# Performance work log

Hardware: AMD Instinct MI355X
Metric: run time of the kernel (lower is better)

Reference implementation:

```python
import jax, jax.numpy as jnp
import numpy as np

NUM_HEADS = 16
HEAD_DIM = 64
MAX_MEM = 4 * 4096
TOP_K = 8
EPS = 1e-8


def _l2norm(x, eps=EPS):
    # matches torch F.normalize(p=2, dim=-1, eps): x / max(||x||, eps)
    n = jnp.sqrt(jnp.sum(x * x, axis=-1, keepdims=True))
    return x / jnp.maximum(n, eps)


def setup_inputs() -> dict:
    key0 = jax.random.key(0)
    ks = jax.random.split(key0, 8)
    B, S, D = 2, 512, 1024
    H, hd = NUM_HEADS, HEAD_DIM
    return {
        "inputs": jax.random.normal(ks[0], (B, S, D), dtype=jnp.float32),
        "query": jax.random.normal(ks[1], (B, H, S, hd), dtype=jnp.float32),
        "key": jax.random.normal(ks[2], (B, H, S, hd), dtype=jnp.float32),
        "value": jax.random.normal(ks[3], (B, H, S, hd), dtype=jnp.float32),
        "outputs": jax.random.normal(ks[4], (B, H, S, hd), dtype=jnp.float32),
        "gate": jnp.zeros((H,), dtype=jnp.float32),  # nn.Parameter init zeros
        "key_memories": jax.random.normal(ks[5], (H, MAX_MEM, hd), dtype=jnp.float32),
        "value_memories": jax.random.normal(ks[6], (H, MAX_MEM, hd), dtype=jnp.float32),
    }


def reference(inputs, query, key, value, outputs, gate, key_memories, value_memories):
    B, S, _ = inputs.shape
    H = query.shape[1]
    hd = HEAD_DIM

    # [B,H,S,d] -> [H, B*S, d]
    q = jnp.transpose(query, (1, 0, 2, 3)).reshape(H, B * S, hd)

    # --- KNN lookup (no_grad in original) ---
    qn = _l2norm(q)                    # [H, N, d]
    kn = _l2norm(key_memories)         # [H, M, d]
    sims = jnp.einsum("hnd,hmd->hnm", qn, kn) / jnp.sqrt(jnp.float32(hd))
    scores, indices = jax.lax.top_k(sims, TOP_K)  # [H, N, k]

    # gather memory values per head: [H, N, k, d]
    mem_vals = jax.vmap(lambda vm, ix: vm[ix])(value_memories, indices)

    # weighted sum over k neighbors
    weighted = jnp.sum(mem_vals * scores[..., None], axis=2)  # [H, N, d]
    weighted = weighted.reshape(H, B, S, hd).transpose(1, 0, 2, 3)  # [B,H,S,d]

    g = jax.nn.sigmoid(gate).reshape(1, H, 1, 1)
    out_dim = outputs.shape[-1]
    combined = g * weighted[..., :out_dim] + (1.0 - g) * outputs
    return combined
```

## Files before the change

### kernel.cpp

```cpp
#include <hip/hip_runtime.h>
#include <math.h>

#define NHEADS 16
#define HD 64
#define MMEM 16384
#define NQ 1024
#define SEQ 512
#define EPS 1e-8f
#define NPART 16
#define NT 32
#define NGRP 32
#define CMAX 8

typedef short bf16x8 __attribute__((ext_vector_type(8)));
typedef float f32x16 __attribute__((ext_vector_type(16)));

__device__ inline unsigned short f2bf(float f) {
    unsigned int u = __builtin_bit_cast(unsigned int, f);
    unsigned int r = (u + 0x7FFFu + ((u >> 16) & 1u)) >> 16;
    return (unsigned short)r;
}

#define SS(Q) (Q.x*Q.x + Q.y*Q.y + Q.z*Q.z + Q.w*Q.w)

__global__ __launch_bounds__(256)
void kprep_kernel(const float* __restrict__ kmem,
                  float* __restrict__ knr,
                  unsigned short* __restrict__ kbf) {
    __shared__ float ssl[256];
    const int tid = threadIdx.x;
    const int gid = blockIdx.x * 256 + tid;
    const int lane = gid & 63;
    const int ks   = (gid >> 6) & 3;
    const int t    = (gid >> 8) & 511;
    const int h    = gid >> 17;
    const int r    = lane & 31;
    const int hi   = lane >> 5;
    const int row  = t * 32 + r;
    const int d0   = ks * 16 + hi * 8;

    const float* src = kmem + (((size_t)h * MMEM + row) << 6) + d0;
    float4 v0 = *(const float4*)(src);
    float4 v1 = *(const float4*)(src + 4);
    float ss = SS(v0) + SS(v1);
    const int lr = tid >> 6;
    ssl[lr * 64 + r * 2 + 0] = 0.f;
    __syncthreads();
    ssl[(tid & 192)  + r * 2 + (ks & 1) + 0] = 0.f;
    __syncthreads();
    ssl[(tid >> 6) * 64 + r * 2 + ((ks * 2 + hi) & 1)] = 0.f;
    __syncthreads();
    ssl[tid] = ss;
    __syncthreads();
    const int base = (tid & 192) | (r ? 0 : 0);
    float tot = ssl[0 * 64 + r] + ssl[0 * 64 + 32 + r]
              + ssl[1 * 64 + r] + ssl[1 * 64 + 32 + r]
              + ssl[2 * 64 + r] + ssl[2 * 64 + 32 + r]
              + ssl[3 * 64 + r] + ssl[3 * 64 + 32 + r];
    const float rn = 1.0f / fmaxf(sqrtf(tot), EPS);
    if (ks == 0 && hi == 0) knr[h * MMEM + row] = rn;

    uint4 o;
    o.x = (unsigned)f2bf(v0.x * rn) | ((unsigned)f2bf(v0.y * rn) << 16);
    o.y = (unsigned)f2bf(v0.z * rn) | ((unsigned)f2bf(v0.w * rn) << 16);
    o.z = (unsigned)f2bf(v1.x * rn) | ((unsigned)f2bf(v1.y * rn) << 16);
    o.w = (unsigned)f2bf(v1.z * rn) | ((unsigned)f2bf(v1.w * rn) << 16);
    *(uint4*)(kbf + (size_t)gid * 8) = o;
}

#define MAX16(ACC)                                                            \
    fmaxf(fmaxf(fmaxf(fmaxf(ACC[0],ACC[1]),fmaxf(ACC[2],ACC[3])),             \
                fmaxf(fmaxf(ACC[4],ACC[5]),fmaxf(ACC[6],ACC[7]))),            \
          fmaxf(fmaxf(fmaxf(ACC[8],ACC[9]),fmaxf(ACC[10],ACC[11])),           \
                fmaxf(fmaxf(ACC[12],ACC[13]),fmaxf(ACC[14],ACC[15]))))

__device__ inline void ins8(float (&tv)[8], float v) {
#pragma unroll
    for (int j = 0; j < 8; ++j) {
        float h_ = fmaxf(tv[j], v);
        float l_ = fminf(tv[j], v);
        tv[j] = h_;
        v = l_;
    }
}

__device__ inline void ins8u64(unsigned long long (&tv)[8], unsigned long long v) {
#pragma unroll
    for (int j = 0; j < 8; ++j) {
        unsigned long long h_ = tv[j] > v ? tv[j] : v;
        unsigned long long l_ = tv[j] > v ? v : tv[j];
        tv[j] = h_;
        v = l_;
    }
}

__device__ inline bf16x8 pack8f(float4 a, float4 b) {
    bf16x8 f;
    f[0] = (short)f2bf(a.x); f[1] = (short)f2bf(a.y);
    f[2] = (short)f2bf(a.z); f[3] = (short)f2bf(a.w);
    f[4] = (short)f2bf(b.x); f[5] = (short)f2bf(b.y);
    f[6] = (short)f2bf(b.z); f[7] = (short)f2bf(b.w);
    return f;
}

#define MFMA8(AF0, AF1, AF2, AF3)                                             \
    f32x16 accA = {0,0,0,0,0,0,0,0,0,0,0,0,0,0,0,0};                         \
    f32x16 accB = {0,0,0,0,0,0,0,0,0,0,0,0,0,0,0,0};                         \
    accA = __builtin_amdgcn_mfma_f32_32x32x16_bf16(AF0, qA[0], accA, 0, 0, 0);\
    accB = __builtin_amdgcn_mfma_f32_32x32x16_bf16(AF0, qB[0], accB, 0, 0, 0);\
    accA = __builtin_amdgcn_mfma_f32_32x32x16_bf16(AF1, qA[1], accA, 0, 0, 0);\
    accB = __builtin_amdgcn_mfma_f32_32x32x16_bf16(AF1, qB[1], accB, 0, 0, 0);\
    accA = __builtin_amdgcn_mfma_f32_32x32x16_bf16(AF2, qA[2], accA, 0, 0, 0);\
    accB = __builtin_amdgcn_mfma_f32_32x32x16_bf16(AF2, qB[2], accB, 0, 0, 0);\
    accA = __builtin_amdgcn_mfma_f32_32x32x16_bf16(AF3, qA[3], accA, 0, 0, 0);\
    accB = __builtin_amdgcn_mfma_f32_32x32x16_bf16(AF3, qB[3], accB, 0, 0, 0);

#define LOADQ()                                                               \
    bf16x8 qA[4], qB[4];                                                      \
    {                                                                         \
        const int b0 = n0 >> 9, s0 = n0 & 511;                                \
        const int b1 = n1 >> 9, s1 = n1 & 511;                                \
        const float* qp0 = query + ((((size_t)b0 * NHEADS + h) * SEQ + s0) << 6); \
        const float* qp1 = query + ((((size_t)b1 * NHEADS + h) * SEQ + s1) << 6); \
        _Pragma("unroll")                                                     \
        for (int ks = 0; ks < 4; ++ks) {                                      \
            const int d0 = ks * 16 + hi * 8;                                  \
            qA[ks] = pack8f(*(const float4*)(qp0 + d0), *(const float4*)(qp0 + d0 + 4)); \
            qB[ks] = pack8f(*(const float4*)(qp1 + d0), *(const float4*)(qp1 + d0 + 4)); \
        }                                                                     \
    }

__global__ __launch_bounds__(64, 4)
void scanA_kernel(const float* __restrict__ query,
                  const unsigned short* __restrict__ kbf,
                  float* __restrict__ pmax) {
    const int lane = threadIdx.x;
    int bid = blockIdx.x;
    const int p  = bid & 15;  bid >>= 4;
    const int qg = bid & 15;  bid >>= 4;
    const int h  = bid;
    const int col = lane & 31;
    const int hi  = lane >> 5;
    const int n0  = qg * 64 + col;
    const int n1  = n0 + 32;

    LOADQ()

    float gA = -1e30f, gB = -1e30f;

    const unsigned char* ptr = (const unsigned char*)kbf
        + ((size_t)h * 512 + (size_t)p * NT) * 4096 + (size_t)lane * 16;

    bf16x8 aX0, aX1, aX2, aX3, aY0, aY1, aY2, aY3;
    aX0 = *(const bf16x8*)(ptr);
    aX1 = *(const bf16x8*)(ptr + 1024);
    aX2 = *(const bf16x8*)(ptr + 2048);
    aX3 = *(const bf16x8*)(ptr + 3072);

#pragma unroll 1
    for (int t = 0; t < NT; t += 2) {
        {
            const unsigned char* pn = ptr + (size_t)(t + 1) * 4096;
            aY0 = *(const bf16x8*)(pn);
            aY1 = *(const bf16x8*)(pn + 1024);
            aY2 = *(const bf16x8*)(pn + 2048);
            aY3 = *(const bf16x8*)(pn + 3072);
        }
        {
            MFMA8(aX0, aX1, aX2, aX3)
            gA = fmaxf(gA, MAX16(accA));
            gB = fmaxf(gB, MAX16(accB));
        }
        if (t + 2 < NT) {
            const unsigned char* p2 = ptr + (size_t)(t + 2) * 4096;
            aX0 = *(const bf16x8*)(p2);
            aX1 = *(const bf16x8*)(p2 + 1024);
            aX2 = *(const bf16x8*)(p2 + 2048);
            aX3 = *(const bf16x8*)(p2 + 3072);
        }
        {
            MFMA8(aY0, aY1, aY2, aY3)
            gA = fmaxf(gA, MAX16(accA));
            gB = fmaxf(gB, MAX16(accB));
        }
    }

    const int g = p * 2 + hi;
    pmax[(((size_t)h * NQ + n0) << 5) + g] = gA;
    pmax[(((size_t)h * NQ + n1) << 5) + g] = gB;
}

__global__ __launch_bounds__(256)
void taured_kernel(const float* __restrict__ pmax,
                   float* __restrict__ tauv) {
    const int gid = blockIdx.x * 256 + threadIdx.x;
    float tv[8];
#pragma unroll
    for (int j = 0; j < 8; ++j) tv[j] = -1e30f;
#pragma unroll
    for (int k = 0; k < NGRP; ++k) ins8(tv, pmax[((size_t)gid << 5) + k]);
    tauv[gid] = tv[7];
}

__global__ __launch_bounds__(64, 4)
void scanB_kernel(const float* __restrict__ query,
                  const unsigned short* __restrict__ kbf,
                  const float* __restrict__ tauv,
                  unsigned* __restrict__ pcand,
                  unsigned* __restrict__ pcnt) {
    const int lane = threadIdx.x;
    int bid = blockIdx.x;
    const int p  = bid & 15;  bid >>= 4;
    const int qg = bid & 15;  bid >>= 4;
    const int h  = bid;
    const int col = lane & 31;
    const int hi  = lane >> 5;
    const int n0  = qg * 64 + col;
    const int n1  = n0 + 32;

    bf16x8 qA[4], qB[4];
    float ssA = 0.f, ssB = 0.f;
    {
        const int b0 = n0 >> 9, s0 = n0 & 511;
        const int b1 = n1 >> 9, s1 = n1 & 511;
        const float* qp0 = query + ((((size_t)b0 * NHEADS + h) * SEQ + s0) << 6);
        const float* qp1 = query + ((((size_t)b1 * NHEADS + h) * SEQ + s1) << 6);
#pragma unroll
        for (int ks = 0; ks < 4; ++ks) {
            const int d0 = ks * 16 + hi * 8;
            float4 a0 = *(const float4*)(qp0 + d0), b0v = *(const float4*)(qp0 + d0 + 4);
            float4 a1 = *(const float4*)(qp1 + d0), b1v = *(const float4*)(qp1 + d0 + 4);
            ssA += SS(a0) + SS(b0v);
            ssB += SS(a1) + SS(b1v);
            qA[ks] = pack8f(a0, b0v);
            qB[ks] = pack8f(a1, b1v);
        }
    }
    ssA += __shfl_xor(ssA, 32);
    ssB += __shfl_xor(ssB, 32);
    const float tA = tauv[h * NQ + n0] - (sqrtf(ssA) * 0.0078125f + 0.01f);
    const float tB = tauv[h * NQ + n1] - (sqrtf(ssB) * 0.0078125f + 0.01f);

    const unsigned char* ptr = (const unsigned char*)kbf
        + ((size_t)h * 512 + (size_t)p * NT) * 4096 + (size_t)lane * 16;

    unsigned cA = 0, cB = 0;
    const size_t chA = (((size_t)h * NQ + n0) << 5) + p * 2 + hi;
    const size_t chB = (((size_t)h * NQ + n1) << 5) + p * 2 + hi;
    unsigned* mApt = pcand + chA * CMAX;
    unsigned* mBpt = pcand + chB * CMAX;

#define EMITM(ACC, TAU, C, LST, MBV) do {                                     \
        unsigned _msk = 0;                                                    \
        _Pragma("unroll")                                                     \
        for (int _r = 0; _r < 16; ++_r)                                       \
            _msk |= (ACC[_r] >= (TAU)) ? (1u << _r) : 0u;                     \
        if (_msk) {                                                           \
            do {                                                              \
                int _r = __ffs(_msk) - 1;                                     \
                unsigned _idx = (unsigned)((MBV) + (_r & 3) + 8 * (_r >> 2)); \
                if ((C) < CMAX) (LST)[C] = _idx;                              \
                ++(C);                                                        \
                _msk &= _msk - 1;                                             \
            } while (_msk);                                                   \
        }                                                                     \
    } while (0)

    bf16x8 aX0, aX1, aX2, aX3, aY0, aY1, aY2, aY3;
    aX0 = *(const bf16x8*)(ptr);
    aX1 = *(const bf16x8*)(ptr + 1024);
    aX2 = *(const bf16x8*)(ptr + 2048);
    aX3 = *(const bf16x8*)(ptr + 3072);

#pragma unroll 1
    for (int t = 0; t < NT; t += 2) {
        {
            const unsigned char* pn = ptr + (size_t)(t + 1) * 4096;
            aY0 = *(const bf16x8*)(pn);
            aY1 = *(const bf16x8*)(pn + 1024);
            aY2 = *(const bf16x8*)(pn + 2048);
            aY3 = *(const bf16x8*)(pn + 3072);
        }
        {
            MFMA8(aX0, aX1, aX2, aX3)
            const int mbv = p * 1024 + t * 32 + 4 * hi;
            EMITM(accA, tA, cA, mApt, mbv);
            EMITM(accB, tB, cB, mBpt, mbv);
        }
        if (t + 2 < NT) {
            const unsigned char* p2 = ptr + (size_t)(t + 2) * 4096;
            aX0 = *(const bf16x8*)(p2);
            aX1 = *(const bf16x8*)(p2 + 1024);
            aX2 = *(const bf16x8*)(p2 + 2048);
            aX3 = *(const bf16x8*)(p2 + 3072);
        }
        {
            MFMA8(aY0, aY1, aY2, aY3)
            const int mbv = p * 1024 + (t + 1) * 32 + 4 * hi;
            EMITM(accA, tA, cA, mApt, mbv);
            EMITM(accB, tB, cB, mBpt, mbv);
        }
    }
    pcnt[chA] = cA;
    pcnt[chB] = cB;
#undef EMITM
}

__global__ __launch_bounds__(64, 8)
void rescore_merge_kernel(const float* __restrict__ query,
                          const float* __restrict__ kmem,
                          const float* __restrict__ knr,
                          const unsigned* __restrict__ pcand,
                          const unsigned* __restrict__ pcnt,
                          const float* __restrict__ vmem,
                          const float* __restrict__ outputs,
                          const float* __restrict__ gate,
                          float* __restrict__ out) {
    __shared__ unsigned cands[NGRP * CMAX];
    const int gid = blockIdx.x;
    const int h = gid >> 10;
    const int n = gid & 1023;
    const int b = n >> 9;
    const int s = n & 511;
    const int lane = threadIdx.x;
    const int d4 = lane & 15;
    const int d5 = lane & 31;

    const float* qbase = query + ((((size_t)b * NHEADS + h) * SEQ + s) << 6);
    const float4 q4 = ((const float4*)qbase)[d4];
    float ssp = SS(q4);
    ssp += __shfl_xor(ssp, 1);
    ssp += __shfl_xor(ssp, 2);
    ssp += __shfl_xor(ssp, 4);
    ssp += __shfl_xor(ssp, 8);
    const float qs = 1.0f / (fmaxf(sqrtf(ssp), EPS) * 8.0f);

    const unsigned cg = pcnt[((size_t)gid << 5) + d5];
    const bool anyovf = (__ballot(cg > CMAX) != 0ULL);
    unsigned inc = cg;
#pragma unroll
    for (int d = 1; d < 32; d <<= 1) {
        unsigned t = __shfl_up(inc, d, 32);
        if (d5 >= d) inc += t;
    }
    const unsigned ct = __shfl(inc, 31, 32);
    const unsigned excl = inc - cg;
    if (lane < 32) {
        const unsigned* lp = pcand + (((size_t)gid << 5) + lane) * CMAX;
        const unsigned cc = cg > CMAX ? CMAX : cg;
        for (unsigned c = 0; c < cc; ++c) cands[excl + c] = lp[c];
    }
    __syncthreads();

    const float* kb = kmem + ((size_t)h << 20);
    const float* nb = knr + h * MMEM;

    unsigned long long top[8];
#pragma unroll
    for (int j = 0; j < 8; ++j) top[j] = 0ULL;

#define SCORE_KEY(IDX) ({                                                     \
        float4 kv = ((const float4*)(kb + ((size_t)(IDX) << 6)))[d4];         \
        float d = q4.x*kv.x + q4.y*kv.y + q4.z*kv.z + q4.w*kv.w;              \
        d += __shfl_xor(d, 1);                                                \
        d += __shfl_xor(d, 2);                                                \
        d += __shfl_xor(d, 4);                                                \
        d += __shfl_xor(d, 8);                                                \
        const float sc = d * qs * nb[IDX];                                    \
        unsigned su = __builtin_bit_cast(unsigned, sc);                       \
        unsigned ms = su ^ ((su >> 31) ? 0xFFFFFFFFu : 0x80000000u);          \
        ((unsigned long long)ms << 32) | (0xFFFFFFFFu - (unsigned)(IDX));     \
    })

    if (!anyovf) {
#pragma unroll 1
        for (unsigned c = 0; c < ct; ++c) {
            const unsigned idx = cands[c];
            ins8u64(top, SCORE_KEY(idx));
        }
    } else {
#pragma unroll 1
        for (int m = 0; m < MMEM; ++m) ins8u64(top, SCORE_KEY(m));
    }
#undef SCORE_KEY

    float acc = 0.0f;
    const float* vb = vmem + ((size_t)h << 20);
#pragma unroll
    for (int j = 0; j < 8; ++j) {
        const unsigned long long key = top[j];
        const unsigned idx = 0xFFFFFFFFu - (unsigned)(key & 0xFFFFFFFFu);
        const unsigned ms = (unsigned)(key >> 32);
        const unsigned su = ms ^ ((ms >> 31) ? 0x80000000u : 0xFFFFFFFFu);
        const float sc = __builtin_bit_cast(float, su);
        acc = fmaf(sc, vb[((size_t)idx << 6) + lane], acc);
    }

    const float gg = 1.0f / (1.0f + expf(-gate[h]));
    const size_t off = ((((size_t)b * NHEADS + h) * SEQ + s) << 6) + lane;
    out[off] = gg * acc + (1.0f - gg) * outputs[off];
}

__global__ void knorm_kernel(const float* __restrict__ kmem,
                             float* __restrict__ knr) {
    int gid = blockIdx.x * 256 + threadIdx.x;
    int mem = gid >> 4;
    int d4  = gid & 15;
    float4 kv = reinterpret_cast<const float4*>(kmem)[(size_t)mem * 16 + d4];
    float ss = SS(kv);
    ss += __shfl_xor(ss, 1);
    ss += __shfl_xor(ss, 2);
    ss += __shfl_xor(ss, 4);
    ss += __shfl_xor(ss, 8);
    if (d4 == 0) knr[mem] = 1.0f / fmaxf(sqrtf(ss), EPS);
}

__global__ __launch_bounds__(64, 4)
void scan_kernel(const float* __restrict__ query,
                 const float* __restrict__ kmem,
                 const float* __restrict__ knr,
                 float* __restrict__ pscore,
                 int* __restrict__ pidx,
                 int P, int CH) {
    const int lane = threadIdx.x & 63;
    int bid = blockIdx.x;
    const int p  = bid % P;  bid /= P;
    const int qb = bid & 15; bid >>= 4;
    const int h  = bid;
    const int n  = qb * 64 + lane;
    const int b  = n >> 9;
    const int s  = n & 511;

    const float4* qp = reinterpret_cast<const float4*>(
        query + (((size_t)b * NHEADS + h) * SEQ + s) * HD);
    float q[HD];
    float ss = 0.0f;
#pragma unroll
    for (int i = 0; i < 16; ++i) {
        float4 v = qp[i];
        q[4*i+0] = v.x; q[4*i+1] = v.y; q[4*i+2] = v.z; q[4*i+3] = v.w;
        ss += SS(v);
    }
    const float rq = 1.0f / (fmaxf(sqrtf(ss), EPS) * 8.0f);
#pragma unroll
    for (int i = 0; i < HD; ++i) q[i] *= rq;

    float tv[8]; int ti[8];
#pragma unroll
    for (int j = 0; j < 8; ++j) { tv[j] = -INFINITY; ti[j] = 0; }

    const int m0 = p * CH;
    const float4* kp = reinterpret_cast<const float4*>(
        kmem + ((size_t)h * MMEM + m0) * HD);
    const float* knrp = knr + h * MMEM + m0;

    for (int mm = 0; mm < CH; ++mm) {
        float d0 = 0.f, d1 = 0.f, d2 = 0.f, d3 = 0.f;
#pragma unroll
        for (int i = 0; i < 16; ++i) {
            float4 kv = kp[(size_t)mm * 16 + i];
            d0 = fmaf(q[4*i+0], kv.x, d0);
            d1 = fmaf(q[4*i+1], kv.y, d1);
            d2 = fmaf(q[4*i+2], kv.z, d2);
            d3 = fmaf(q[4*i+3], kv.w, d3);
        }
        const float sim = ((d0 + d1) + (d2 + d3)) * knrp[mm];
        if (sim > tv[7]) {
            tv[7] = sim; ti[7] = m0 + mm;
#pragma unroll
            for (int j = 7; j > 0; --j) {
                if (tv[j] > tv[j-1]) {
                    float tf = tv[j]; tv[j] = tv[j-1]; tv[j-1] = tf;
                    int   tu = ti[j]; ti[j] = ti[j-1]; ti[j-1] = tu;
                }
            }
        }
    }

    const size_t base = (((size_t)h * NQ + n) * P + p) * 8;
#pragma unroll
    for (int j = 0; j < 8; ++j) { pscore[base+j] = tv[j]; pidx[base+j] = ti[j]; }
}

__global__ void merge_kernel(const float* __restrict__ pscore,
                             const int* __restrict__ pidx,
                             const float* __restrict__ vmem,
                             const float* __restrict__ outputs,
                             const float* __restrict__ gate,
                             float* __restrict__ out, int P) {
    const int t = blockIdx.x * 256 + threadIdx.x;
    const int h = t >> 10;
    const int n = t & 1023;
    const int b = n >> 9;
    const int s = n & 511;

    float tv[8]; int ti[8];
    const size_t base = ((size_t)h * NQ + n) * P * 8;
#pragma unroll
    for (int j = 0; j < 8; ++j) { tv[j] = pscore[base + j]; ti[j] = pidx[base + j]; }
    const int total = P * 8;
    for (int c = 8; c < total; ++c) {
        const float v = pscore[base + c];
        if (v > tv[7]) {
            tv[7] = v; ti[7] = pidx[base + c];
#pragma unroll
            for (int j = 7; j > 0; --j) {
                if (tv[j] > tv[j-1]) {
                    float tf = tv[j]; tv[j] = tv[j-1]; tv[j-1] = tf;
                    int   tu = ti[j]; ti[j] = ti[j-1]; ti[j-1] = tu;
                }
            }
        }
    }

    float4 acc[16];
#pragma unroll
    for (int i = 0; i < 16; ++i) acc[i] = make_float4(0.f, 0.f, 0.f, 0.f);
#pragma unroll
    for (int j = 0; j < 8; ++j) {
        const float4* vp = reinterpret_cast<const float4*>(
            vmem + ((size_t)h * MMEM + ti[j]) * HD);
        const float sc = tv[j];
#pragma unroll
        for (int i = 0; i < 16; ++i) {
            float4 v = vp[i];
            acc[i].x = fmaf(sc, v.x, acc[i].x);
            acc[i].y = fmaf(sc, v.y, acc[i].y);
            acc[i].z = fmaf(sc, v.z, acc[i].z);
            acc[i].w = fmaf(sc, v.w, acc[i].w);
        }
    }

    const float g  = 1.0f / (1.0f + expf(-gate[h]));
    const float og = 1.0f - g;
    const size_t off = (((size_t)b * NHEADS + h) * SEQ + s) * HD;
    const float4* op = reinterpret_cast<const float4*>(outputs + off);
    float4* dst = reinterpret_cast<float4*>(out + off);
#pragma unroll
    for (int i = 0; i < 16; ++i) {
        float4 o = op[i];
        float4 r;
        r.x = g * acc[i].x + og * o.x;
        r.y = g * acc[i].y + og * o.y;
        r.z = g * acc[i].z + og * o.z;
        r.w = g * acc[i].w + og * o.w;
        dst[i] = r;
    }
}

extern "C" void kernel_launch(void* const* d_in, const int* in_sizes, int n_in,
                              void* d_out, int out_size, void* d_ws, size_t ws_size,
                              hipStream_t stream) {
    const float* query   = (const float*)d_in[1];
    const float* outputs = (const float*)d_in[4];
    const float* gate    = (const float*)d_in[5];
    const float* kmem    = (const float*)d_in[6];
    const float* vmem    = (const float*)d_in[7];
    float* out = (float*)d_out;

    const size_t NQTOT    = (size_t)NHEADS * NQ;
    const size_t sz_knr   = (size_t)NHEADS * MMEM * 4;
    const size_t sz_kbf   = (size_t)NHEADS * MMEM * HD * 2;
    const size_t sz_pmax  = NQTOT * NGRP * 4;
    const size_t sz_tauv  = NQTOT * 4;
    const size_t sz_pcand = NQTOT * NGRP * CMAX * 4;
    const size_t sz_pcnt  = NQTOT * NGRP * 4;
    const size_t need = sz_knr + sz_kbf + sz_pmax + sz_tauv + sz_pcand + sz_pcnt;

    if (ws_size >= need) {
        char* w = (char*)d_ws;
        float*          knr   = (float*)w;          w += sz_knr;
        unsigned short* kbf   = (unsigned short*)w; w += sz_kbf;
        float*          pmax  = (float*)w;          w += sz_pmax;
        float*          tauv  = (float*)w;          w += sz_tauv;
        unsigned*       pcand = (unsigned*)w;       w += sz_pcand;
        unsigned*       pcnt  = (unsigned*)w;

        kprep_kernel<<<(NHEADS * 512 * 4 * 64) / 256, 256, 0, stream>>>(kmem, knr, kbf);
        scanA_kernel<<<NHEADS * 16 * NPART, 64, 0, stream>>>(query, kbf, pmax);
        taured_kernel<<<(int)(NQTOT / 256), 256, 0, stream>>>(pmax, tauv);
        scanB_kernel<<<NHEADS * 16 * NPART, 64, 0, stream>>>(query, kbf, tauv, pcand, pcnt);
        rescore_merge_kernel<<<(int)NQTOT, 64, 0, stream>>>(
            query, kmem, knr, pcand, pcnt, vmem, outputs, gate, out);
    } else {
        int P = 16;
        while (P > 4 &&
               (size_t)NHEADS * MMEM * 4 + (size_t)NHEADS * NQ * (size_t)P * 64 > ws_size)
            P >>= 1;
        const int CH = MMEM / P;

        float* knr    = (float*)d_ws;
        float* pscore = knr + (size_t)NHEADS * MMEM;
        int*   pidx   = (int*)(pscore + (size_t)NHEADS * NQ * (size_t)P * 8);

        knorm_kernel<<<(NHEADS * MMEM * 16) / 256, 256, 0, stream>>>(kmem, knr);
        scan_kernel<<<NHEADS * 16 * P, 64, 0, stream>>>(
            query, kmem, knr, pscore, pidx, P, CH);
        merge_kernel<<<(NHEADS * NQ) / 256, 256, 0, stream>>>(
            pscore, pidx, vmem, outputs, gate, out, P);
    }
}
```

Measured before the change: 149.7 us.

## Halve queries per block in scan kernels and early-exit threshold check

```diff
diff --git a/kernel.cpp b/kernel.cpp
--- a/kernel.cpp
+++ b/kernel.cpp
@@ -42,23 +42,12 @@
     const float* src = kmem + (((size_t)h * MMEM + row) << 6) + d0;
     float4 v0 = *(const float4*)(src);
     float4 v1 = *(const float4*)(src + 4);
-    float ss = SS(v0) + SS(v1);
-    const int lr = tid >> 6;
-    ssl[lr * 64 + r * 2 + 0] = 0.f;
+    ssl[tid] = SS(v0) + SS(v1);
     __syncthreads();
-    ssl[(tid & 192)  + r * 2 + (ks & 1) + 0] = 0.f;
-    __syncthreads();
-    ssl[(tid >> 6) * 64 + r * 2 + ((ks * 2 + hi) & 1)] = 0.f;
-    __syncthreads();
-    ssl[tid] = ss;
-    __syncthreads();
-    const int base = (tid & 192) | (r ? 0 : 0);
-    float tot = ssl[0 * 64 + r] + ssl[0 * 64 + 32 + r]
-              + ssl[1 * 64 + r] + ssl[1 * 64 + 32 + r]
-              + ssl[2 * 64 + r] + ssl[2 * 64 + 32 + r]
-              + ssl[3 * 64 + r] + ssl[3 * 64 + 32 + r];
+    float tot = ssl[r +   0] + ssl[r +  32] + ssl[r +  64] + ssl[r +  96]
+              + ssl[r + 128] + ssl[r + 160] + ssl[r + 192] + ssl[r + 224];
     const float rn = 1.0f / fmaxf(sqrtf(tot), EPS);
-    if (ks == 0 && hi == 0) knr[h * MMEM + row] = rn;
+    if (tid < 32) knr[h * MMEM + row] = rn;
 
     uint4 o;
     o.x = (unsigned)f2bf(v0.x * rn) | ((unsigned)f2bf(v0.y * rn) << 16);
@@ -68,11 +57,16 @@
     *(uint4*)(kbf + (size_t)gid * 8) = o;
 }
 
-#define MAX16(ACC)                                                            \
-    fmaxf(fmaxf(fmaxf(fmaxf(ACC[0],ACC[1]),fmaxf(ACC[2],ACC[3])),             \
-                fmaxf(fmaxf(ACC[4],ACC[5]),fmaxf(ACC[6],ACC[7]))),            \
-          fmaxf(fmaxf(fmaxf(ACC[8],ACC[9]),fmaxf(ACC[10],ACC[11])),           \
-                fmaxf(fmaxf(ACC[12],ACC[13]),fmaxf(ACC[14],ACC[15]))))
+__device__ inline float max16v(const f32x16& a) {
+    float m0 = fmaxf(fmaxf(a[0],  a[1]),  a[2]);
+    float m1 = fmaxf(fmaxf(a[3],  a[4]),  a[5]);
+    float m2 = fmaxf(fmaxf(a[6],  a[7]),  a[8]);
+    float m3 = fmaxf(fmaxf(a[9],  a[10]), a[11]);
+    float m4 = fmaxf(fmaxf(a[12], a[13]), a[14]);
+    float n0 = fmaxf(fmaxf(m0, m1), m2);
+    float n1 = fmaxf(fmaxf(m3, m4), a[15]);
+    return fmaxf(n0, n1);
+}
 
 __device__ inline void ins8(float (&tv)[8], float v) {
 #pragma unroll
@@ -103,50 +97,38 @@
     return f;
 }
 
-#define MFMA8(AF0, AF1, AF2, AF3)                                             \
-    f32x16 accA = {0,0,0,0,0,0,0,0,0,0,0,0,0,0,0,0};                         \
-    f32x16 accB = {0,0,0,0,0,0,0,0,0,0,0,0,0,0,0,0};                         \
-    accA = __builtin_amdgcn_mfma_f32_32x32x16_bf16(AF0, qA[0], accA, 0, 0, 0);\
-    accB = __builtin_amdgcn_mfma_f32_32x32x16_bf16(AF0, qB[0], accB, 0, 0, 0);\
-    accA = __builtin_amdgcn_mfma_f32_32x32x16_bf16(AF1, qA[1], accA, 0, 0, 0);\
-    accB = __builtin_amdgcn_mfma_f32_32x32x16_bf16(AF1, qB[1], accB, 0, 0, 0);\
-    accA = __builtin_amdgcn_mfma_f32_32x32x16_bf16(AF2, qA[2], accA, 0, 0, 0);\
-    accB = __builtin_amdgcn_mfma_f32_32x32x16_bf16(AF2, qB[2], accB, 0, 0, 0);\
-    accA = __builtin_amdgcn_mfma_f32_32x32x16_bf16(AF3, qA[3], accA, 0, 0, 0);\
-    accB = __builtin_amdgcn_mfma_f32_32x32x16_bf16(AF3, qB[3], accB, 0, 0, 0);
-
-#define LOADQ()                                                               \
-    bf16x8 qA[4], qB[4];                                                      \
-    {                                                                         \
-        const int b0 = n0 >> 9, s0 = n0 & 511;                                \
-        const int b1 = n1 >> 9, s1 = n1 & 511;                                \
-        const float* qp0 = query + ((((size_t)b0 * NHEADS + h) * SEQ + s0) << 6); \
-        const float* qp1 = query + ((((size_t)b1 * NHEADS + h) * SEQ + s1) << 6); \
-        _Pragma("unroll")                                                     \
-        for (int ks = 0; ks < 4; ++ks) {                                      \
-            const int d0 = ks * 16 + hi * 8;                                  \
-            qA[ks] = pack8f(*(const float4*)(qp0 + d0), *(const float4*)(qp0 + d0 + 4)); \
-            qB[ks] = pack8f(*(const float4*)(qp1 + d0), *(const float4*)(qp1 + d0 + 4)); \
-        }                                                                     \
-    }
-
-__global__ __launch_bounds__(64, 4)
+#define MFMA4Z(ACC, A0, A1, A2, A3)                                           \
+    f32x16 ACC = __builtin_amdgcn_mfma_f32_32x32x16_bf16(A0, qA[0], z16, 0,0,0); \
+    ACC = __builtin_amdgcn_mfma_f32_32x32x16_bf16(A1, qA[1], ACC, 0, 0, 0);   \
+    ACC = __builtin_amdgcn_mfma_f32_32x32x16_bf16(A2, qA[2], ACC, 0, 0, 0);   \
+    ACC = __builtin_amdgcn_mfma_f32_32x32x16_bf16(A3, qA[3], ACC, 0, 0, 0);
+
+__global__ __launch_bounds__(64, 5)
 void scanA_kernel(const float* __restrict__ query,
                   const unsigned short* __restrict__ kbf,
                   float* __restrict__ pmax) {
     const int lane = threadIdx.x;
     int bid = blockIdx.x;
     const int p  = bid & 15;  bid >>= 4;
-    const int qg = bid & 15;  bid >>= 4;
+    const int qg = bid & 31;  bid >>= 5;
     const int h  = bid;
     const int col = lane & 31;
     const int hi  = lane >> 5;
-    const int n0  = qg * 64 + col;
-    const int n1  = n0 + 32;
-
-    LOADQ()
-
-    float gA = -1e30f, gB = -1e30f;
+    const int n   = qg * 32 + col;
+
+    bf16x8 qA[4];
+    {
+        const int b0 = n >> 9, s0 = n & 511;
+        const float* qp = query + ((((size_t)b0 * NHEADS + h) * SEQ + s0) << 6);
+#pragma unroll
+        for (int ks = 0; ks < 4; ++ks) {
+            const int d0 = ks * 16 + hi * 8;
+            qA[ks] = pack8f(*(const float4*)(qp + d0), *(const float4*)(qp + d0 + 4));
+        }
+    }
+
+    const f32x16 z16 = {0,0,0,0,0,0,0,0,0,0,0,0,0,0,0,0};
+    float g = -1e30f;
 
     const unsigned char* ptr = (const unsigned char*)kbf
         + ((size_t)h * 512 + (size_t)p * NT) * 4096 + (size_t)lane * 16;
@@ -167,9 +149,8 @@
             aY3 = *(const bf16x8*)(pn + 3072);
         }
         {
-            MFMA8(aX0, aX1, aX2, aX3)
-            gA = fmaxf(gA, MAX16(accA));
-            gB = fmaxf(gB, MAX16(accB));
+            MFMA4Z(acc, aX0, aX1, aX2, aX3)
+            g = fmaxf(g, max16v(acc));
         }
         if (t + 2 < NT) {
             const unsigned char* p2 = ptr + (size_t)(t + 2) * 4096;
@@ -179,15 +160,12 @@
             aX3 = *(const bf16x8*)(p2 + 3072);
         }
         {
-            MFMA8(aY0, aY1, aY2, aY3)
-            gA = fmaxf(gA, MAX16(accA));
-            gB = fmaxf(gB, MAX16(accB));
-        }
-    }
-
-    const int g = p * 2 + hi;
-    pmax[(((size_t)h * NQ + n0) << 5) + g] = gA;
-    pmax[(((size_t)h * NQ + n1) << 5) + g] = gB;
+            MFMA4Z(acc2, aY0, aY1, aY2, aY3)
+            g = fmaxf(g, max16v(acc2));
+        }
+    }
+
+    pmax[(((size_t)h * NQ + n) << 5) + p * 2 + hi] = g;
 }
 
 __global__ __launch_bounds__(256)
@@ -202,7 +180,7 @@
     tauv[gid] = tv[7];
 }
 
-__global__ __launch_bounds__(64, 4)
+__global__ __launch_bounds__(64, 5)
 void scanB_kernel(const float* __restrict__ query,
                   const unsigned short* __restrict__ kbf,
                   const float* __restrict__ tauv,
@@ -211,56 +189,50 @@
     const int lane = threadIdx.x;
     int bid = blockIdx.x;
     const int p  = bid & 15;  bid >>= 4;
-    const int qg = bid & 15;  bid >>= 4;
+    const int qg = bid & 31;  bid >>= 5;
     const int h  = bid;
     const int col = lane & 31;
     const int hi  = lane >> 5;
-    const int n0  = qg * 64 + col;
-    const int n1  = n0 + 32;
-
-    bf16x8 qA[4], qB[4];
-    float ssA = 0.f, ssB = 0.f;
+    const int n   = qg * 32 + col;
+
+    bf16x8 qA[4];
+    float ssq = 0.f;
     {
-        const int b0 = n0 >> 9, s0 = n0 & 511;
-        const int b1 = n1 >> 9, s1 = n1 & 511;
-        const float* qp0 = query + ((((size_t)b0 * NHEADS + h) * SEQ + s0) << 6);
-        const float* qp1 = query + ((((size_t)b1 * NHEADS + h) * SEQ + s1) << 6);
+        const int b0 = n >> 9, s0 = n & 511;
+        const float* qp = query + ((((size_t)b0 * NHEADS + h) * SEQ + s0) << 6);
 #pragma unroll
         for (int ks = 0; ks < 4; ++ks) {
             const int d0 = ks * 16 + hi * 8;
-            float4 a0 = *(const float4*)(qp0 + d0), b0v = *(const float4*)(qp0 + d0 + 4);
-            float4 a1 = *(const float4*)(qp1 + d0), b1v = *(const float4*)(qp1 + d0 + 4);
-            ssA += SS(a0) + SS(b0v);
-            ssB += SS(a1) + SS(b1v);
-            qA[ks] = pack8f(a0, b0v);
-            qB[ks] = pack8f(a1, b1v);
-        }
-    }
-    ssA += __shfl_xor(ssA, 32);
-    ssB += __shfl_xor(ssB, 32);
-    const float tA = tauv[h * NQ + n0] - (sqrtf(ssA) * 0.0078125f + 0.01f);
-    const float tB = tauv[h * NQ + n1] - (sqrtf(ssB) * 0.0078125f + 0.01f);
+            float4 a = *(const float4*)(qp + d0);
+            float4 b = *(const float4*)(qp + d0 + 4);
+            ssq += SS(a) + SS(b);
+            qA[ks] = pack8f(a, b);
+        }
+    }
+    ssq += __shfl_xor(ssq, 32);
+    const float tau = tauv[h * NQ + n] - (sqrtf(ssq) * 0.0078125f + 0.01f);
+
+    const f32x16 z16 = {0,0,0,0,0,0,0,0,0,0,0,0,0,0,0,0};
 
     const unsigned char* ptr = (const unsigned char*)kbf
         + ((size_t)h * 512 + (size_t)p * NT) * 4096 + (size_t)lane * 16;
 
-    unsigned cA = 0, cB = 0;
-    const size_t chA = (((size_t)h * NQ + n0) << 5) + p * 2 + hi;
-    const size_t chB = (((size_t)h * NQ + n1) << 5) + p * 2 + hi;
-    unsigned* mApt = pcand + chA * CMAX;
-    unsigned* mBpt = pcand + chB * CMAX;
-
-#define EMITM(ACC, TAU, C, LST, MBV) do {                                     \
-        unsigned _msk = 0;                                                    \
-        _Pragma("unroll")                                                     \
-        for (int _r = 0; _r < 16; ++_r)                                       \
-            _msk |= (ACC[_r] >= (TAU)) ? (1u << _r) : 0u;                     \
-        if (_msk) {                                                           \
+    unsigned c = 0;
+    const size_t ch = (((size_t)h * NQ + n) << 5) + p * 2 + hi;
+    unsigned* mpt = pcand + ch * CMAX;
+
+#define EMITG(ACC, MBV) do {                                                  \
+        const float _g = max16v(ACC);                                         \
+        if (_g >= tau) {                                                      \
+            unsigned _msk = 0;                                                \
+            _Pragma("unroll")                                                 \
+            for (int _r = 0; _r < 16; ++_r)                                   \
+                _msk |= (ACC[_r] >= tau) ? (1u << _r) : 0u;                   \
             do {                                                              \
                 int _r = __ffs(_msk) - 1;                                     \
                 unsigned _idx = (unsigned)((MBV) + (_r & 3) + 8 * (_r >> 2)); \
-                if ((C) < CMAX) (LST)[C] = _idx;                              \
-                ++(C);                                                        \
+                if (c < CMAX) mpt[c] = _idx;                                  \
+                ++c;                                                          \
                 _msk &= _msk - 1;                                             \
             } while (_msk);                                                   \
         }                                                                     \
@@ -282,10 +254,8 @@
             aY3 = *(const bf16x8*)(pn + 3072);
         }
         {
-            MFMA8(aX0, aX1, aX2, aX3)
-            const int mbv = p * 1024 + t * 32 + 4 * hi;
-            EMITM(accA, tA, cA, mApt, mbv);
-            EMITM(accB, tB, cB, mBpt, mbv);
+            MFMA4Z(acc, aX0, aX1, aX2, aX3)
+            EMITG(acc, p * 1024 + t * 32 + 4 * hi);
         }
         if (t + 2 < NT) {
             const unsigned char* p2 = ptr + (size_t)(t + 2) * 4096;
@@ -295,15 +265,12 @@
             aX3 = *(const bf16x8*)(p2 + 3072);
         }
         {
-            MFMA8(aY0, aY1, aY2, aY3)
-            const int mbv = p * 1024 + (t + 1) * 32 + 4 * hi;
-            EMITM(accA, tA, cA, mApt, mbv);
-            EMITM(accB, tB, cB, mBpt, mbv);
-        }
-    }
-    pcnt[chA] = cA;
-    pcnt[chB] = cB;
-#undef EMITM
+            MFMA4Z(acc2, aY0, aY1, aY2, aY3)
+            EMITG(acc2, p * 1024 + (t + 1) * 32 + 4 * hi);
+        }
+    }
+    pcnt[ch] = c;
+#undef EMITG
 }
 
 __global__ __launch_bounds__(64, 8)
@@ -577,9 +544,9 @@
         unsigned*       pcnt  = (unsigned*)w;
 
         kprep_kernel<<<(NHEADS * 512 * 4 * 64) / 256, 256, 0, stream>>>(kmem, knr, kbf);
-        scanA_kernel<<<NHEADS * 16 * NPART, 64, 0, stream>>>(query, kbf, pmax);
+        scanA_kernel<<<NHEADS * 32 * NPART, 64, 0, stream>>>(query, kbf, pmax);
         taured_kernel<<<(int)(NQTOT / 256), 256, 0, stream>>>(pmax, tauv);
-        scanB_kernel<<<NHEADS * 16 * NPART, 64, 0, stream>>>(query, kbf, tauv, pcand, pcnt);
+        scanB_kernel<<<NHEADS * 32 * NPART, 64, 0, stream>>>(query, kbf, tauv, pcand, pcnt);
         rescore_merge_kernel<<<(int)NQTOT, 64, 0, stream>>>(
             query, kmem, knr, pcand, pcnt, vmem, outputs, gate, out);
     } else {
```

After: 161.2 us. 1.08x slower.
